# Optimization experiments

Measured on AMD Instinct MI355X. Metric: run time of the kernel, lower is better.

Reference implementation:

```python
import jax, jax.numpy as jnp
import numpy as np

E = 256      # embed_dim
S = 64       # seq_len (decode steps)
T = 512      # signal length
B = 128      # batch
LN_EPS = 1e-5


def setup_inputs() -> dict:
    key = jax.random.key(0)
    ks = jax.random.split(key, 12)
    sc = 1.0 / np.sqrt(E)
    sc2 = 1.0 / np.sqrt(2 * E)
    signal = jax.random.normal(ks[0], (B, T, E), jnp.float32)
    bases = jax.random.normal(ks[1], (B, S, E), jnp.float32)
    padding_mask = jax.random.uniform(ks[2], (B, T)) < 0.3  # bool
    return {
        "signal": signal,
        "bases": bases,
        "padding_mask": padding_mask,
        # attention projection W: Linear(E, E)
        "W_w": jax.random.uniform(ks[3], (E, E), jnp.float32, -sc, sc),
        "W_b": jax.random.uniform(ks[4], (E,), jnp.float32, -sc, sc),
        # LayerNorm(2E)
        "ln_g": jnp.ones((2 * E,), jnp.float32),
        "ln_b": jnp.zeros((2 * E,), jnp.float32),
        # GRUCell(2E -> E), torch layout: [3E, in] with gate order r,z,n
        "gru_w_ih": jax.random.uniform(ks[5], (3 * E, 2 * E), jnp.float32, -sc, sc),
        "gru_b_ih": jax.random.uniform(ks[6], (3 * E,), jnp.float32, -sc, sc),
        "gru_w_hh": jax.random.uniform(ks[7], (3 * E, E), jnp.float32, -sc, sc),
        "gru_b_hh": jax.random.uniform(ks[8], (3 * E,), jnp.float32, -sc, sc),
        "hidden_init": jnp.zeros((E,), jnp.float32),
    }


def _layernorm(x, g, b):
    mu = jnp.mean(x, axis=-1, keepdims=True)
    var = jnp.mean(jnp.square(x - mu), axis=-1, keepdims=True)
    return (x - mu) * jax.lax.rsqrt(var + LN_EPS) * g + b


def reference(signal, bases, padding_mask, W_w, W_b, ln_g, ln_b,
              gru_w_ih, gru_b_ih, gru_w_hh, gru_b_hh, hidden_init):
    attn_mask = jnp.where(padding_mask, -jnp.inf, 0.0).astype(signal.dtype)  # [B,T]

    def step(h, x_i):
        # attention: query = W(h)
        v = h @ W_w.T + W_b                                  # [B,E]
        e = jnp.einsum('be,bte->bt', v, signal) + attn_mask   # [B,T]
        score = jax.nn.softmax(e, axis=-1)                    # [B,T]
        context = jnp.einsum('bt,bte->be', score, signal)     # [B,E]
        inp = jnp.concatenate([x_i, context], axis=-1)        # [B,2E]
        inp = _layernorm(inp, ln_g, ln_b)
        # GRUCell (torch gate order r, z, n)
        gx = inp @ gru_w_ih.T + gru_b_ih                      # [B,3E]
        gh = h @ gru_w_hh.T + gru_b_hh                        # [B,3E]
        xr, xz, xn = jnp.split(gx, 3, axis=-1)
        hr, hz, hn = jnp.split(gh, 3, axis=-1)
        r = jax.nn.sigmoid(xr + hr)
        z = jax.nn.sigmoid(xz + hz)
        n = jnp.tanh(xn + r * hn)
        h_new = (1.0 - z) * n + z * h
        return h_new, h_new

    h0 = jnp.broadcast_to(hidden_init, (bases.shape[0], hidden_init.shape[0]))
    xs = jnp.swapaxes(bases, 0, 1)          # [S,B,E]
    _, outs = jax.lax.scan(step, h0, xs)     # [S,B,E]
    return jnp.swapaxes(outs, 0, 1)          # [B,S,E]
```

## Files before the change

kernel.cpp:

```cpp
#include <hip/hip_runtime.h>

#define EDIM 256
#define SLEN 64
#define TLEN 512
#define NT 1024
#define NWAVES 16
#define JH 128
#define WA_ROWS 640
#define GX_ROWS 384
#define SIG_LDS_T 96
#define WSCALE 262144.0f
#define WINV (1.0f / 262144.0f)

__global__ __launch_bounds__(256) void pack_fused_i16_kernel(
    const float* __restrict__ Ww, const float* __restrict__ whh,
    const float* __restrict__ wih, short* __restrict__ WA16, short* __restrict__ wX16)
{
    const int z = blockIdx.z;
    const float* in; short* out; int R, C, ostride, ooff;
    if (z < 12) {
        int mat = z / 6, rem = z % 6, role = rem / 3, g = rem % 3;
        if (mat == 0) {
            in = whh + (size_t)(g * 256 + role * JH) * 256; C = 256;
            out = WA16 + (size_t)role * 256 * WA_ROWS; ostride = WA_ROWS; ooff = 256 + g * JH; R = JH;
        } else {
            in = wih + (size_t)(g * 256 + role * JH) * 512; C = 512;
            out = wX16 + (size_t)role * 512 * GX_ROWS; ostride = GX_ROWS; ooff = g * JH; R = JH;
        }
    } else {
        int role = z - 12; in = Ww; C = 256;
        out = WA16 + (size_t)role * 256 * WA_ROWS; ostride = WA_ROWS; ooff = 0; R = 256;
    }
    const int r0 = blockIdx.y * 64, c0 = blockIdx.x * 64;
    if (r0 >= R || c0 >= C) return;
    __shared__ float tile[64][65];
    for (int i = threadIdx.x; i < 64 * 64; i += 256) {
        int r = i >> 6, c = i & 63;
        tile[r][c] = in[(size_t)(r0 + r) * C + (c0 + c)];
    }
    __syncthreads();
    for (int i = threadIdx.x; i < 64 * 64; i += 256) {
        int c = i >> 6, r = i & 63;
        int q = __float2int_rn(tile[r][c] * WSCALE);
        q = q > 32767 ? 32767 : (q < -32768 ? -32768 : q);
        out[(size_t)(c0 + c) * ostride + ooff + (r0 + r)] = (short)q;
    }
}

__global__ __launch_bounds__(NT) void gru_decoder_kernel(
    const float* __restrict__ signal,
    const float* __restrict__ bases,
    const int* __restrict__ mask,
    const short* __restrict__ WA16,
    const float* __restrict__ Wb,
    const float* __restrict__ lng, const float* __restrict__ lnb,
    const short* __restrict__ wX16,
    const float* __restrict__ bih, const float* __restrict__ bhh,
    const float* __restrict__ hinit,
    unsigned long long* __restrict__ payload,
    float* __restrict__ out, int nb)
{
    const int bid  = blockIdx.x;
    const int pair = bid % nb;
    const int role = bid / nb;
    const int b    = pair;
    const int joff = role * JH;
    const int tid  = threadIdx.x;
    const int lane = tid & 63;
    const int wv   = tid >> 6;
    const int rot  = (bid & 7) << 3;

    __shared__ float sig_lds[SIG_LDS_T * EDIM];
    __shared__ float h_s[EDIM];
    __shared__ float wap[4 * WA_ROWS];
    __shared__ float ctxp[NWAVES * EDIM];
    __shared__ float mw_s[NWAVES], lw_s[NWAVES];
    __shared__ float inp_s[2 * EDIM], inpn_s[2 * EDIM];
    __shared__ float gxp[8 * GX_ROWS];
    __shared__ float embias_s[TLEN];
    __shared__ float scr2[2 * NWAVES];
    __shared__ float sWb[EDIM], sbih[768], sbhh[768], slng[512], slnb[512];

    const short* WAr  = WA16 + (size_t)role * 256 * WA_ROWS;
    const short* wXr  = wX16 + (size_t)role * 512 * GX_ROWS;
    const float* sigb = signal + (size_t)b * TLEN * EDIM;
    const int*  maskb = mask + (size_t)b * TLEN;

    unsigned long long* pbuf = payload + (size_t)pair * 512;

    if (tid < 256) { h_s[tid] = hinit[tid]; sWb[tid] = Wb[tid]; }
    if (tid < 512) { embias_s[tid] = maskb[tid] ? -1e30f : 0.0f; slng[tid] = lng[tid]; slnb[tid] = lnb[tid]; }
    if (tid < 768) { sbih[tid] = bih[tid]; sbhh[tid] = bhh[tid]; }
    for (int i = tid; i < SIG_LDS_T * EDIM / 4; i += NT) {
        *reinterpret_cast<float4*>(&sig_lds[i * 4]) =
            *reinterpret_cast<const float4*>(sigb + (size_t)i * 4);
    }
    __syncthreads();

    for (int s = 0; s < SLEN; ++s) {
        {
            const int q = tid >> 8;
            const int w = tid & 255;
            if (w < 160) {
                const int r4 = w * 4;
                const short* base = WAr + (size_t)(q * 64) * WA_ROWS + r4;
                const float* xk = &h_s[q * 64];
                float a0 = 0.f, a1 = 0.f, a2 = 0.f, a3 = 0.f;
#pragma unroll 8
                for (int kk = 0; kk < 64; ++kk) {
                    const int k = (kk + rot) & 63;
                    short4 w4 = *reinterpret_cast<const short4*>(base + (size_t)k * WA_ROWS);
                    float x = xk[k];
                    a0 += (float)w4.x * x; a1 += (float)w4.y * x;
                    a2 += (float)w4.z * x; a3 += (float)w4.w * x;
                }
                float4 acc; acc.x = a0 * WINV; acc.y = a1 * WINV; acc.z = a2 * WINV; acc.w = a3 * WINV;
                *reinterpret_cast<float4*>(&wap[q * WA_ROWS + r4]) = acc;
            } else {
                const int li = q * 96 + (w - 160);
                if (li < 256) inp_s[li] = bases[((size_t)b * SLEN + s) * EDIM + li];
            }
        }
        __syncthreads();

        {
            float4 wb = *reinterpret_cast<const float4*>(&sWb[lane * 4]);
            float4 p0 = *reinterpret_cast<const float4*>(&wap[0 * WA_ROWS + lane * 4]);
            float4 p1 = *reinterpret_cast<const float4*>(&wap[1 * WA_ROWS + lane * 4]);
            float4 p2 = *reinterpret_cast<const float4*>(&wap[2 * WA_ROWS + lane * 4]);
            float4 p3 = *reinterpret_cast<const float4*>(&wap[3 * WA_ROWS + lane * 4]);
            float4 v4;
            v4.x = wb.x + p0.x + p1.x + p2.x + p3.x;
            v4.y = wb.y + p0.y + p1.y + p2.y + p3.y;
            v4.z = wb.z + p0.z + p1.z + p2.z + p3.z;
            v4.w = wb.w + p0.w + p1.w + p2.w + p3.w;

            float m = -3e38f, l = 0.f;
            float c0 = 0.f, c1 = 0.f, c2 = 0.f, c3 = 0.f;
            const int t0 = wv * 32;

            auto flash = [&](auto fetch) {
#pragma unroll 4
                for (int i = 0; i < 32; i += 2) {
                    const int ta = t0 + i, tb = ta + 1;
                    float4 A  = fetch(ta);
                    float4 Bv = fetch(tb);
                    float da = A.x * v4.x + A.y * v4.y + A.z * v4.z + A.w * v4.w;
                    float db = Bv.x * v4.x + Bv.y * v4.y + Bv.z * v4.z + Bv.w * v4.w;
#pragma unroll
                    for (int mk = 32; mk > 0; mk >>= 1) {
                        da += __shfl_xor(da, mk, 64);
                        db += __shfl_xor(db, mk, 64);
                    }
                    float ea = da + embias_s[ta];
                    float eb = db + embias_s[tb];
                    float mn = fmaxf(m, fmaxf(ea, eb));
                    float sc = __expf(m - mn);
                    float pa = __expf(ea - mn);
                    float pb = __expf(eb - mn);
                    l  = l  * sc + pa + pb;
                    c0 = c0 * sc + pa * A.x + pb * Bv.x;
                    c1 = c1 * sc + pa * A.y + pb * Bv.y;
                    c2 = c2 * sc + pa * A.z + pb * Bv.z;
                    c3 = c3 * sc + pa * A.w + pb * Bv.w;
                    m = mn;
                }
            };
            if (wv < 3) {
                flash([&](int t) {
                    return *reinterpret_cast<const float4*>(&sig_lds[t * EDIM + lane * 4]);
                });
            } else {
                flash([&](int t) {
                    return *reinterpret_cast<const float4*>(sigb + (size_t)t * EDIM + lane * 4);
                });
            }
            if (lane == 0) { mw_s[wv] = m; lw_s[wv] = l; }
            float4 cc; cc.x = c0; cc.y = c1; cc.z = c2; cc.w = c3;
            *reinterpret_cast<float4*>(&ctxp[wv * EDIM + lane * 4]) = cc;
        }
        __syncthreads();

        if (tid < EDIM) {
            float M = mw_s[0];
#pragma unroll
            for (int w = 1; w < NWAVES; ++w) M = fmaxf(M, mw_s[w]);
            float L = 0.f, c = 0.f;
#pragma unroll
            for (int w = 0; w < NWAVES; ++w) {
                float ew = __expf(mw_s[w] - M);
                L += lw_s[w] * ew;
                c += ctxp[w * EDIM + tid] * ew;
            }
            inp_s[EDIM + tid] = c / L;
        }
        __syncthreads();

        {
            float val = (tid < 2 * EDIM) ? inp_s[tid] : 0.f;
            float s1 = val, s2 = val * val;
#pragma unroll
            for (int mk = 32; mk > 0; mk >>= 1) {
                s1 += __shfl_xor(s1, mk, 64);
                s2 += __shfl_xor(s2, mk, 64);
            }
            if (lane == 0) { scr2[wv] = s1; scr2[NWAVES + wv] = s2; }
            __syncthreads();
            float S1 = 0.f, S2 = 0.f;
#pragma unroll
            for (int w = 0; w < NWAVES; ++w) { S1 += scr2[w]; S2 += scr2[NWAVES + w]; }
            float mu  = S1 * (1.0f / (2 * EDIM));
            float var = S2 * (1.0f / (2 * EDIM)) - mu * mu;
            float rs  = rsqrtf(var + 1e-5f);
            if (tid < 2 * EDIM) inpn_s[tid] = (val - mu) * rs * slng[tid] + slnb[tid];
        }
        __syncthreads();

        {
            const int q = tid >> 7;
            const int w = tid & 127;
            if (w < 96) {
                const int r4 = w * 4;
                const short* base = wXr + (size_t)(q * 64) * GX_ROWS + r4;
                const float* xk = &inpn_s[q * 64];
                float a0 = 0.f, a1 = 0.f, a2 = 0.f, a3 = 0.f;
#pragma unroll 8
                for (int kk = 0; kk < 64; ++kk) {
                    const int k = (kk + rot) & 63;
                    short4 w4 = *reinterpret_cast<const short4*>(base + (size_t)k * GX_ROWS);
                    float x = xk[k];
                    a0 += (float)w4.x * x; a1 += (float)w4.y * x;
                    a2 += (float)w4.z * x; a3 += (float)w4.w * x;
                }
                float4 acc; acc.x = a0 * WINV; acc.y = a1 * WINV; acc.z = a2 * WINV; acc.w = a3 * WINV;
                *reinterpret_cast<float4*>(&gxp[q * GX_ROWS + r4]) = acc;
            }
        }
        __syncthreads();

        {
            unsigned long long* myslot = pbuf + (s & 1) * 256 + role * JH;
            unsigned long long* pslot  = pbuf + (s & 1) * 256 + (1 - role) * JH;
            if (tid < JH) {
                const int jl = tid, j = joff + jl;
                float xr = sbih[j], xz = sbih[EDIM + j], xn = sbih[2 * EDIM + j];
#pragma unroll
                for (int q = 0; q < 8; ++q) {
                    xr += gxp[q * GX_ROWS + jl];
                    xz += gxp[q * GX_ROWS + JH + jl];
                    xn += gxp[q * GX_ROWS + 2 * JH + jl];
                }
                float hr = sbhh[j], hz = sbhh[EDIM + j], hn_ = sbhh[2 * EDIM + j];
#pragma unroll
                for (int q = 0; q < 4; ++q) {
                    hr  += wap[q * WA_ROWS + 256 + jl];
                    hz  += wap[q * WA_ROWS + 384 + jl];
                    hn_ += wap[q * WA_ROWS + 512 + jl];
                }
                float r = 1.0f / (1.0f + __expf(-(xr + hr)));
                float z = 1.0f / (1.0f + __expf(-(xz + hz)));
                float n = tanhf(xn + r * hn_);
                float hnew = (1.0f - z) * n + z * h_s[j];
                h_s[j] = hnew;
                out[((size_t)b * SLEN + s) * EDIM + j] = hnew;

                const unsigned int want = (unsigned int)(s + 1);
                unsigned long long wrd = ((unsigned long long)want << 32)
                                       | (unsigned long long)__float_as_uint(hnew);
                __hip_atomic_store(myslot + jl, wrd, __ATOMIC_RELAXED, __HIP_MEMORY_SCOPE_AGENT);
                unsigned long long pw;
                for (;;) {
                    pw = __hip_atomic_load(pslot + jl, __ATOMIC_RELAXED, __HIP_MEMORY_SCOPE_AGENT);
                    if ((unsigned int)(pw >> 32) >= want) break;
                    __builtin_amdgcn_s_sleep(1);
                }
                h_s[(JH - joff) + jl] = __uint_as_float((unsigned int)pw);
            }
        }
        __syncthreads();
    }
}

extern "C" void kernel_launch(void* const* d_in, const int* in_sizes, int n_in,
                              void* d_out, int out_size, void* d_ws, size_t ws_size,
                              hipStream_t stream) {
    const float* signal = (const float*)d_in[0];
    const float* bases  = (const float*)d_in[1];
    const int*   mask   = (const int*)d_in[2];
    const float* Ww     = (const float*)d_in[3];
    const float* Wb     = (const float*)d_in[4];
    const float* lng    = (const float*)d_in[5];
    const float* lnb    = (const float*)d_in[6];
    const float* wih    = (const float*)d_in[7];
    const float* bih    = (const float*)d_in[8];
    const float* whh    = (const float*)d_in[9];
    const float* bhh    = (const float*)d_in[10];
    const float* hinit  = (const float*)d_in[11];
    float*       out    = (float*)d_out;

    const int B = in_sizes[0] / (TLEN * EDIM);

    short* WA16 = (short*)d_ws;
    short* wX16 = WA16 + 2 * 256 * WA_ROWS;
    unsigned long long* payload =
        (unsigned long long*)((char*)d_ws + 2 * 256 * WA_ROWS * 2 + 2 * 512 * GX_ROWS * 2);

    hipMemsetAsync(payload, 0, (size_t)B * 512 * sizeof(unsigned long long), stream);
    pack_fused_i16_kernel<<<dim3(8, 4, 14), 256, 0, stream>>>(Ww, whh, wih, WA16, wX16);
    gru_decoder_kernel<<<dim3(2 * B), dim3(NT), 0, stream>>>(
        signal, bases, mask, WA16, Wb, lng, lnb, wX16, bih, bhh, hinit, payload, out, B);
}
```

Measured before the change: 1.928 ms.

## Quantize signal to int16 and double LDS-resident signal rows

Adds a pre-pass that converts the fp32 signal into int16 fixed point with a scale of 4096. The decoder then keeps 192 timesteps in LDS instead of 96 and reads the rest from global memory at half the bytes. Scale factors are folded into the query vector and the context output. The rotated k-loop start in the matvecs is also removed. The cost is an extra full pass over the signal each call plus quantization error in the attention scores and context.

```diff
diff --git a/kernel.cpp b/kernel.cpp
--- a/kernel.cpp
+++ b/kernel.cpp
@@ -8,9 +8,11 @@
 #define JH 128
 #define WA_ROWS 640
 #define GX_ROWS 384
-#define SIG_LDS_T 96
+#define SIG_LDS_T 192
 #define WSCALE 262144.0f
 #define WINV (1.0f / 262144.0f)
+#define SSCALE 4096.0f
+#define SINV (1.0f / 4096.0f)
 
 __global__ __launch_bounds__(256) void pack_fused_i16_kernel(
     const float* __restrict__ Ww, const float* __restrict__ whh,
@@ -47,8 +49,24 @@
     }
 }
 
+__global__ __launch_bounds__(256) void sig_i16_kernel(
+    const float* __restrict__ in, short* __restrict__ out, int n4)
+{
+    int i = blockIdx.x * 256 + threadIdx.x;
+    if (i >= n4) return;
+    float4 v = *reinterpret_cast<const float4*>(in + (size_t)i * 4);
+    int a = __float2int_rn(v.x * SSCALE), b = __float2int_rn(v.y * SSCALE);
+    int c = __float2int_rn(v.z * SSCALE), d = __float2int_rn(v.w * SSCALE);
+    a = a > 32767 ? 32767 : (a < -32768 ? -32768 : a);
+    b = b > 32767 ? 32767 : (b < -32768 ? -32768 : b);
+    c = c > 32767 ? 32767 : (c < -32768 ? -32768 : c);
+    d = d > 32767 ? 32767 : (d < -32768 ? -32768 : d);
+    short4 o; o.x = (short)a; o.y = (short)b; o.z = (short)c; o.w = (short)d;
+    *reinterpret_cast<short4*>(out + (size_t)i * 4) = o;
+}
+
 __global__ __launch_bounds__(NT) void gru_decoder_kernel(
-    const float* __restrict__ signal,
+    const short* __restrict__ sigh,
     const float* __restrict__ bases,
     const int* __restrict__ mask,
     const short* __restrict__ WA16,
@@ -68,9 +86,8 @@
     const int tid  = threadIdx.x;
     const int lane = tid & 63;
     const int wv   = tid >> 6;
-    const int rot  = (bid & 7) << 3;
-
-    __shared__ float sig_lds[SIG_LDS_T * EDIM];
+
+    __shared__ short sig_lds[SIG_LDS_T * EDIM];
     __shared__ float h_s[EDIM];
     __shared__ float wap[4 * WA_ROWS];
     __shared__ float ctxp[NWAVES * EDIM];
@@ -83,7 +100,7 @@
 
     const short* WAr  = WA16 + (size_t)role * 256 * WA_ROWS;
     const short* wXr  = wX16 + (size_t)role * 512 * GX_ROWS;
-    const float* sigb = signal + (size_t)b * TLEN * EDIM;
+    const short* sgb  = sigh + (size_t)b * TLEN * EDIM;
     const int*  maskb = mask + (size_t)b * TLEN;
 
     unsigned long long* pbuf = payload + (size_t)pair * 512;
@@ -91,9 +108,9 @@
     if (tid < 256) { h_s[tid] = hinit[tid]; sWb[tid] = Wb[tid]; }
     if (tid < 512) { embias_s[tid] = maskb[tid] ? -1e30f : 0.0f; slng[tid] = lng[tid]; slnb[tid] = lnb[tid]; }
     if (tid < 768) { sbih[tid] = bih[tid]; sbhh[tid] = bhh[tid]; }
-    for (int i = tid; i < SIG_LDS_T * EDIM / 4; i += NT) {
-        *reinterpret_cast<float4*>(&sig_lds[i * 4]) =
-            *reinterpret_cast<const float4*>(sigb + (size_t)i * 4);
+    for (int i = tid; i < SIG_LDS_T * EDIM / 8; i += NT) {
+        *reinterpret_cast<uint4*>(&sig_lds[i * 8]) =
+            *reinterpret_cast<const uint4*>(sgb + (size_t)i * 8);
     }
     __syncthreads();
 
@@ -107,8 +124,7 @@
                 const float* xk = &h_s[q * 64];
                 float a0 = 0.f, a1 = 0.f, a2 = 0.f, a3 = 0.f;
 #pragma unroll 8
-                for (int kk = 0; kk < 64; ++kk) {
-                    const int k = (kk + rot) & 63;
+                for (int k = 0; k < 64; ++k) {
                     short4 w4 = *reinterpret_cast<const short4*>(base + (size_t)k * WA_ROWS);
                     float x = xk[k];
                     a0 += (float)w4.x * x; a1 += (float)w4.y * x;
@@ -130,15 +146,19 @@
             float4 p2 = *reinterpret_cast<const float4*>(&wap[2 * WA_ROWS + lane * 4]);
             float4 p3 = *reinterpret_cast<const float4*>(&wap[3 * WA_ROWS + lane * 4]);
             float4 v4;
-            v4.x = wb.x + p0.x + p1.x + p2.x + p3.x;
-            v4.y = wb.y + p0.y + p1.y + p2.y + p3.y;
-            v4.z = wb.z + p0.z + p1.z + p2.z + p3.z;
-            v4.w = wb.w + p0.w + p1.w + p2.w + p3.w;
+            v4.x = (wb.x + p0.x + p1.x + p2.x + p3.x) * SINV;
+            v4.y = (wb.y + p0.y + p1.y + p2.y + p3.y) * SINV;
+            v4.z = (wb.z + p0.z + p1.z + p2.z + p3.z) * SINV;
+            v4.w = (wb.w + p0.w + p1.w + p2.w + p3.w) * SINV;
 
             float m = -3e38f, l = 0.f;
             float c0 = 0.f, c1 = 0.f, c2 = 0.f, c3 = 0.f;
             const int t0 = wv * 32;
 
+            auto cvt4 = [](short4 w) {
+                float4 f; f.x = (float)w.x; f.y = (float)w.y; f.z = (float)w.z; f.w = (float)w.w;
+                return f;
+            };
             auto flash = [&](auto fetch) {
 #pragma unroll 4
                 for (int i = 0; i < 32; i += 2) {
@@ -166,13 +186,13 @@
                     m = mn;
                 }
             };
-            if (wv < 3) {
+            if (wv < 6) {
                 flash([&](int t) {
-                    return *reinterpret_cast<const float4*>(&sig_lds[t * EDIM + lane * 4]);
+                    return cvt4(*reinterpret_cast<const short4*>(&sig_lds[t * EDIM + lane * 4]));
                 });
             } else {
                 flash([&](int t) {
-                    return *reinterpret_cast<const float4*>(sigb + (size_t)t * EDIM + lane * 4);
+                    return cvt4(*reinterpret_cast<const short4*>(sgb + (size_t)t * EDIM + lane * 4));
                 });
             }
             if (lane == 0) { mw_s[wv] = m; lw_s[wv] = l; }
@@ -192,7 +212,7 @@
                 L += lw_s[w] * ew;
                 c += ctxp[w * EDIM + tid] * ew;
             }
-            inp_s[EDIM + tid] = c / L;
+            inp_s[EDIM + tid] = (c / L) * SINV;
         }
         __syncthreads();
 
@@ -225,8 +245,7 @@
                 const float* xk = &inpn_s[q * 64];
                 float a0 = 0.f, a1 = 0.f, a2 = 0.f, a3 = 0.f;
 #pragma unroll 8
-                for (int kk = 0; kk < 64; ++kk) {
-                    const int k = (kk + rot) & 63;
+                for (int k = 0; k < 64; ++k) {
                     short4 w4 = *reinterpret_cast<const short4*>(base + (size_t)k * GX_ROWS);
                     float x = xk[k];
                     a0 += (float)w4.x * x; a1 += (float)w4.y * x;
@@ -304,9 +323,12 @@
     short* wX16 = WA16 + 2 * 256 * WA_ROWS;
     unsigned long long* payload =
         (unsigned long long*)((char*)d_ws + 2 * 256 * WA_ROWS * 2 + 2 * 512 * GX_ROWS * 2);
+    short* sigh = (short*)(payload + (size_t)B * 512);
 
     hipMemsetAsync(payload, 0, (size_t)B * 512 * sizeof(unsigned long long), stream);
     pack_fused_i16_kernel<<<dim3(8, 4, 14), 256, 0, stream>>>(Ww, whh, wih, WA16, wX16);
+    const int n4 = B * TLEN * EDIM / 4;
+    sig_i16_kernel<<<dim3((n4 + 255) / 256), 256, 0, stream>>>(signal, sigh, n4);
     gru_decoder_kernel<<<dim3(2 * B), dim3(NT), 0, stream>>>(
-        signal, bases, mask, WA16, Wb, lng, lnb, wX16, bih, bhh, hinit, payload, out, B);
+        sigh, bases, mask, WA16, Wb, lng, lnb, wX16, bih, bhh, hinit, payload, out, B);
 }
```

New measurement: 1.911 ms. Within noise of the previous version (-0.9%).
